# Optimization experiments

Hardware: AMD Instinct MI355X
Metric: run time of the kernel (lower is better)

Reference implementation:

```python
import math
import jax, jax.numpy as jnp
import numpy as np

B, S, D, H = 2, 2048, 1024, 16


def setup_inputs() -> dict:
    key = jax.random.key(0)
    ks = jax.random.split(key, 8)
    scale = 1.0 / math.sqrt(D)
    kv_mask = jax.random.randint(ks[1], (B, S), 0, 2).astype(bool)
    kv_mask = kv_mask.at[:, 0].set(True)  # ensure at least one valid kv per batch
    return {
        "q": jax.random.normal(ks[0], (B, S, D), dtype=jnp.float32),
        "kv_mask": kv_mask,
        "Wq": jax.random.normal(ks[2], (D, D), dtype=jnp.float32) * scale,
        "Wk": jax.random.normal(ks[3], (D, D), dtype=jnp.float32) * scale,
        "Wv": jax.random.normal(ks[4], (D, D), dtype=jnp.float32) * scale,
        "Wo": jax.random.normal(ks[5], (D, D), dtype=jnp.float32) * scale,
        "bo": jax.random.normal(ks[6], (D,), dtype=jnp.float32) * 0.01,
        "num_heads": H,
    }


def _pass_with_mask(x, W, mask, b=None):
    # Linear applied everywhere, output zeroed where mask is False (pass_with_mask)
    y = x @ W.T
    if b is not None:
        y = y + b
    return jnp.where(mask[..., None], y, 0.0)


def reference(q, kv_mask, Wq, Wk, Wv, Wo, bo, num_heads):
    b, s, d = q.shape
    hd = d // num_heads
    q_mask = jnp.ones((b, s), dtype=bool)  # default q_mask in the module
    # self-attention: k = v = q
    qh = _pass_with_mask(q, Wq, q_mask).reshape(b, s, num_heads, hd)
    kh = _pass_with_mask(q, Wk, kv_mask).reshape(b, s, num_heads, hd)
    vh = _pass_with_mask(q, Wv, kv_mask).reshape(b, s, num_heads, hd)
    # scores: note the module scales by sqrt(model_dim), NOT sqrt(head_dim)
    scores = jnp.einsum("bqhd,bkhd->bhqk", qh, kh) / math.sqrt(d)
    mask = (q_mask[:, :, None] & kv_mask[:, None, :])[:, None, :, :]  # [b,1,q,k]
    scores = jnp.where(mask, scores, -jnp.inf)
    attn = jax.nn.softmax(scores, axis=-1)
    attn = jnp.where(mask, attn, 0.0)
    out = jnp.einsum("bhqk,bkhd->bqhd", attn, vh).reshape(b, s, d)
    return _pass_with_mask(out, Wo, q_mask, bo)
```

## Files before the change

### kernel.cpp

```cpp
#include <hip/hip_runtime.h>
#include <math.h>

#define B_ 2
#define S_ 2048
#define DM 1024
#define NH 16
#define HD 64

typedef unsigned short u16;
typedef unsigned int u32;
typedef __attribute__((ext_vector_type(8))) short bf16x8;
typedef __attribute__((ext_vector_type(4))) float f32x4;

#define C2SCALE 0.0450842200277800f

__device__ __forceinline__ u16 f2bf(float x) {
  unsigned u = __float_as_uint(x);
  u = (u + 0x7FFFu + ((u >> 16) & 1u)) >> 16;
  return (u16)u;
}

__device__ __forceinline__ u32 cvtpk(float lo, float hi) {
  u32 r;
  asm("v_cvt_pk_bf16_f32 %0, %1, %2" : "=v"(r) : "v"(lo), "v"(hi));
  return r;
}

__device__ __forceinline__ float exp2a(float x) {
  float r;
  asm("v_exp_f32 %0, %1" : "=v"(r) : "v"(x));
  return r;
}

__device__ __forceinline__ void gload_lds16(const u16* g, u16* l) {
  __builtin_amdgcn_global_load_lds((const __attribute__((address_space(1))) void*)g,
                                   (__attribute__((address_space(3))) void*)l, 16, 0, 0);
}

__device__ __forceinline__ int sigpos(int w6) {
  return ((w6 >> 5) << 5) | (((w6 >> 2) & 3) << 3) | (((w6 >> 4) & 1) << 2) | (w6 & 3);
}

__global__ void cvt_all(const float* __restrict__ q, const float* __restrict__ Wq,
                        const float* __restrict__ Wk, const float* __restrict__ Wv,
                        const float* __restrict__ Wo, const int* __restrict__ kvm,
                        u16* __restrict__ Xbf, u16* __restrict__ Wcat,
                        u16* __restrict__ Wobf, u16* __restrict__ mwg) {
  const int NQ4 = (B_ * S_ * DM) / 4;
  const int NW4 = (DM * DM) / 4;
  const int total = NQ4 + 4 * NW4;
  int i = blockIdx.x * blockDim.x + threadIdx.x;
  int stride = gridDim.x * blockDim.x;
  for (int t = i; t < B_ * S_; t += stride) {
    int kv = t & (S_ - 1);
    mwg[(t & ~(S_ - 1)) + (kv & ~63) + sigpos(kv & 63)] = kvm[t] ? 0xFFFFu : 0u;
  }
  for (; i < total; i += stride) {
    const float* src;
    u16* dst;
    if (i < NQ4) {
      src = q + (size_t)i * 4; dst = Xbf + (size_t)i * 4;
    } else {
      int t = i - NQ4;
      if (t < NW4)            { src = Wq + (size_t)t * 4; dst = Wcat + (size_t)t * 4; }
      else if (t < 2 * NW4)   { src = Wk + (size_t)(t - NW4) * 4;     dst = Wcat + DM * DM + (size_t)(t - NW4) * 4; }
      else if (t < 3 * NW4)   { src = Wv + (size_t)(t - 2 * NW4) * 4; dst = Wcat + 2 * DM * DM + (size_t)(t - 2 * NW4) * 4; }
      else                    { src = Wo + (size_t)(t - 3 * NW4) * 4; dst = Wobf + (size_t)(t - 3 * NW4) * 4; }
    }
    float4 v = *(const float4*)src;
    ushort4 o;
    o.x = f2bf(v.x); o.y = f2bf(v.y); o.z = f2bf(v.z); o.w = f2bf(v.w);
    *(ushort4*)dst = o;
  }
}

template <int MODE>
__global__ __launch_bounds__(256, 2) void gemm_bt(
    const u16* __restrict__ A, const u16* __restrict__ Bw, int K,
    u16* __restrict__ qo, u16* __restrict__ ko, u16* __restrict__ vo,
    float* __restrict__ fo, const float* __restrict__ bias, int N) {
  __shared__ __align__(16) u16 As[128 * 32];
  __shared__ __align__(16) u16 Bs[128 * 32];
  const int tid = threadIdx.x;
  const int wv = tid >> 6, lane = tid & 63;
  const int g = lane >> 4, c = lane & 15;
  const int wr = wv >> 1, wc = wv & 1;
  const int L = blockIdx.y * gridDim.x + blockIdx.x;
  const int cpx = (gridDim.x * gridDim.y) >> 3;
  const int Ls = (L & 7) * cpx + (L >> 3);
  const int Mb = (Ls & 31) << 7, Nb = (Ls >> 5) << 7;

  f32x4 acc[4][4];
#pragma unroll
  for (int i = 0; i < 4; i++)
#pragma unroll
    for (int j = 0; j < 4; j++) acc[i][j] = f32x4{0.f, 0.f, 0.f, 0.f};

  for (int kb = 0; kb < K; kb += 32) {
#pragma unroll
    for (int it = 0; it < 2; ++it) {
      int id = it * 256 + tid;
      int m = id >> 2, kk = (id & 3) * 8;
      gload_lds16(A + (size_t)(Mb + m) * K + kb + kk, As + (it * 4 + wv) * 512);
      gload_lds16(Bw + (size_t)(Nb + m) * K + kb + kk, Bs + (it * 4 + wv) * 512);
    }
    __syncthreads();
    bf16x8 af[4], bfr[4];
#pragma unroll
    for (int mi = 0; mi < 4; mi++)
      af[mi] = *(const bf16x8*)(As + (wr * 64 + mi * 16 + c) * 32 + g * 8);
#pragma unroll
    for (int ni = 0; ni < 4; ni++)
      bfr[ni] = *(const bf16x8*)(Bs + (wc * 64 + ni * 16 + c) * 32 + g * 8);
#pragma unroll
    for (int mi = 0; mi < 4; mi++)
#pragma unroll
      for (int ni = 0; ni < 4; ni++)
        acc[mi][ni] = __builtin_amdgcn_mfma_f32_16x16x32_bf16(af[mi], bfr[ni], acc[mi][ni], 0, 0, 0);
    __syncthreads();
  }

  if (MODE == 0) {
#pragma unroll
    for (int mi = 0; mi < 4; mi++) {
#pragma unroll
      for (int ni = 0; ni < 4; ni++) {
        int n = Nb + wc * 64 + ni * 16 + c;
        int which = n >> 10, nn = n & 1023;
        int h = nn >> 6, d = nn & 63;
        int row0 = Mb + wr * 64 + mi * 16 + g * 4;
        int b0 = row0 >> 11, s0 = row0 & 2047;
        if (which == 2) {
          int pos = sigpos(s0 & 63);
          uint2 o;
          o.x = cvtpk(acc[mi][ni][0], acc[mi][ni][1]);
          o.y = cvtpk(acc[mi][ni][2], acc[mi][ni][3]);
          *(uint2*)(vo + ((size_t)((b0 * NH + h) * HD + d)) * S_ + (s0 & ~63) + pos) = o;
        } else if (which == 0) {
#pragma unroll
          for (int r = 0; r < 4; r++)
            qo[(((size_t)(b0 * NH + h)) * S_ + s0 + r) * HD + d] =
                f2bf(acc[mi][ni][r] * C2SCALE);
        } else {
#pragma unroll
          for (int r = 0; r < 4; r++)
            ko[(((size_t)(b0 * NH + h)) * S_ + s0 + r) * HD + d] = f2bf(acc[mi][ni][r]);
        }
      }
    }
  } else {
#pragma unroll
    for (int mi = 0; mi < 4; mi++) {
#pragma unroll
      for (int ni = 0; ni < 4; ni++) {
        int n = Nb + wc * 64 + ni * 16 + c;
        float bv = bias[n];
#pragma unroll
        for (int r = 0; r < 4; r++) {
          int row = Mb + wr * 64 + mi * 16 + g * 4 + r;
          fo[(size_t)row * N + n] = acc[mi][ni][r] + bv;
        }
      }
    }
  }
}

__global__ __launch_bounds__(512, 4) void attn_kernel(
    const u16* __restrict__ qb, const u16* __restrict__ kb,
    const u16* __restrict__ vtb, const u16* __restrict__ mwg,
    u16* __restrict__ ob) {
  __shared__ __align__(16) u16 Kl[2][64 * 64];
  __shared__ __align__(16) u16 Vl[2][64 * 64];
  __shared__ __align__(16) u16 MW[S_];

  const int tid = threadIdx.x;
  const int wv = tid >> 6, lane = tid & 63;
  const int g = lane >> 4, c = lane & 15;

  const int L = blockIdx.x;
  const int j = L >> 3;
  const int bh = ((L & 7) << 2) | (j >> 4);
  const int qi = j & 15;
  const int b = bh >> 4, h = bh & 15;
  const int q0 = qi * 128;
  const size_t bhbase = (size_t)bh * (S_ * HD);

  ((uint2*)MW)[tid] = ((const uint2*)(mwg + b * S_))[tid];

  bf16x8 qf[2];
#pragma unroll
  for (int ks = 0; ks < 2; ks++)
    qf[ks] = *(const bf16x8*)(qb + bhbase + (size_t)(q0 + wv * 16 + c) * HD + ks * 32 + g * 8);

  f32x4 Oa[4];
#pragma unroll
  for (int di = 0; di < 4; di++) Oa[di] = f32x4{0.f, 0.f, 0.f, 0.f};
  f32x4 lacc = f32x4{0.f, 0.f, 0.f, 0.f};

  union { u32 u[4]; bf16x8 v; } ones;
#pragma unroll
  for (int w = 0; w < 4; w++) ones.u[w] = 0x3F803F80u;

  const int srow = tid >> 3;
  const int scol8 = tid & 7;
  const u16* kg = kb + bhbase + (size_t)srow * HD + scol8 * 8;
  const u16* vg = vtb + bhbase + (size_t)srow * S_ + scol8 * 8;
  const int wslot = scol8 ^ (srow & 7);
  u16* kld = &Kl[0][srow * 64 + wslot * 8];
  u16* vld = &Vl[0][srow * 64 + wslot * 8];

  bf16x8 krg = *(const bf16x8*)kg;
  bf16x8 vrg = *(const bf16x8*)vg;
  *(bf16x8*)kld = krg;
  *(bf16x8*)vld = vrg;
  krg = *(const bf16x8*)(kg + 64 * HD);
  vrg = *(const bf16x8*)(vg + 64);
  __syncthreads();

  const int swz = c & 7;
  const int NT = 32;

  for (int t = 0; t < NT; ++t) {
    const int cur = t & 1;
    if (t + 1 < NT) {
      *(bf16x8*)(kld + (cur ^ 1) * 4096) = krg;
      *(bf16x8*)(vld + (cur ^ 1) * 4096) = vrg;
      if (t + 2 < NT) {
        krg = *(const bf16x8*)(kg + (t + 2) * (64 * HD));
        vrg = *(const bf16x8*)(vg + (t + 2) * 64);
      }
    }
    const u16* KB = &Kl[cur][0];
    const u16* VB = &Vl[cur][0];

    f32x4 Sa[4];
#pragma unroll
    for (int ni = 0; ni < 4; ni++) Sa[ni] = f32x4{0.f, 0.f, 0.f, 0.f};
    __builtin_amdgcn_s_setprio(1);
#pragma unroll
    for (int ks = 0; ks < 2; ks++) {
      bf16x8 kf[4];
#pragma unroll
      for (int ni = 0; ni < 4; ni++)
        kf[ni] = *(const bf16x8*)&KB[(ni * 16 + c) * 64 + (((4 * ks + g) ^ swz) * 8)];
#pragma unroll
      for (int ni = 0; ni < 4; ni++)
        Sa[ni] = __builtin_amdgcn_mfma_f32_16x16x32_bf16(kf[ni], qf[ks], Sa[ni], 0, 0, 0);
    }
    __builtin_amdgcn_s_setprio(0);

    bf16x8 Pa[2];
#pragma unroll
    for (int ks = 0; ks < 2; ks++) {
      uint4 mw = *(const uint4*)&MW[t * 64 + ks * 32 + g * 8];
      union { u32 u[4]; bf16x8 v; } pw;
      pw.u[0] = cvtpk(exp2a(Sa[2 * ks][0]), exp2a(Sa[2 * ks][1])) & mw.x;
      pw.u[1] = cvtpk(exp2a(Sa[2 * ks][2]), exp2a(Sa[2 * ks][3])) & mw.y;
      pw.u[2] = cvtpk(exp2a(Sa[2 * ks + 1][0]), exp2a(Sa[2 * ks + 1][1])) & mw.z;
      pw.u[3] = cvtpk(exp2a(Sa[2 * ks + 1][2]), exp2a(Sa[2 * ks + 1][3])) & mw.w;
      Pa[ks] = pw.v;
    }

    __builtin_amdgcn_s_setprio(1);
    lacc = __builtin_amdgcn_mfma_f32_16x16x32_bf16(ones.v, Pa[0], lacc, 0, 0, 0);
    lacc = __builtin_amdgcn_mfma_f32_16x16x32_bf16(ones.v, Pa[1], lacc, 0, 0, 0);
#pragma unroll
    for (int ks = 0; ks < 2; ks++) {
      bf16x8 vf[4];
#pragma unroll
      for (int di = 0; di < 4; di++)
        vf[di] = *(const bf16x8*)&VB[(di * 16 + c) * 64 + (((4 * ks + g) ^ swz) * 8)];
#pragma unroll
      for (int di = 0; di < 4; di++)
        Oa[di] = __builtin_amdgcn_mfma_f32_16x16x32_bf16(vf[di], Pa[ks], Oa[di], 0, 0, 0);
    }
    __builtin_amdgcn_s_setprio(0);

    __syncthreads();
  }

  float inv = 1.f / lacc[0];
  int q = q0 + wv * 16 + c;
  size_t base = ((size_t)(b * S_ + q)) * DM + (size_t)h * HD;
#pragma unroll
  for (int di = 0; di < 4; di++) {
    uint2 o;
    o.x = cvtpk(Oa[di][0] * inv, Oa[di][1] * inv);
    o.y = cvtpk(Oa[di][2] * inv, Oa[di][3] * inv);
    *(uint2*)(ob + base + di * 16 + g * 4) = o;
  }
}

extern "C" void kernel_launch(void* const* d_in, const int* in_sizes, int n_in,
                              void* d_out, int out_size, void* d_ws, size_t ws_size,
                              hipStream_t stream) {
  const float* q  = (const float*)d_in[0];
  const int* kvm  = (const int*)d_in[1];
  const float* Wq = (const float*)d_in[2];
  const float* Wk = (const float*)d_in[3];
  const float* Wv = (const float*)d_in[4];
  const float* Wo = (const float*)d_in[5];
  const float* bo = (const float*)d_in[6];
  float* out = (float*)d_out;
  char* ws = (char*)d_ws;

  u16* Xbf   = (u16*)(ws);
  u16* Wcat  = (u16*)(ws + (8u << 20));
  u16* Wobf  = (u16*)(ws + (14u << 20));
  u16* qbuf  = (u16*)(ws + (16u << 20));
  u16* kbuf  = (u16*)(ws + (24u << 20));
  u16* vtbuf = (u16*)(ws + (32u << 20));
  u16* mwg   = (u16*)(ws + (40u << 20));
  u16* obuf  = Xbf;

  cvt_all<<<2048, 256, 0, stream>>>(q, Wq, Wk, Wv, Wo, kvm, Xbf, Wcat, Wobf, mwg);
  gemm_bt<0><<<dim3(32, 24), 256, 0, stream>>>(Xbf, Wcat, DM, qbuf, kbuf, vtbuf,
                                               nullptr, nullptr, 3 * DM);
  attn_kernel<<<512, 512, 0, stream>>>(qbuf, kbuf, vtbuf, mwg, obuf);
  gemm_bt<1><<<dim3(32, 8), 256, 0, stream>>>(obuf, Wobf, DM, nullptr, nullptr,
                                              nullptr, out, bo, DM);
}
```

Baseline: 113.9 us.

## Double attention KV tile to 128 keys and split output GEMM into 128x64 tiles

The attention kernel now stages 128-key K/V tiles per iteration (16 iterations instead of 32), halving the number of barriers and pipeline steps while doubling LDS per buffer. The output projection gets a dedicated 128x64-tile GEMM with 512 blocks instead of 256 128x128 blocks, giving more blocks to fill the CUs on the small final GEMM. The cost is higher LDS use per attention block, which may reduce occupancy, and more register pressure from eight score accumulators.

Result: no change. 112.2 us (-1.5%).

```diff
diff --git a/kernel.cpp b/kernel.cpp
--- a/kernel.cpp
+++ b/kernel.cpp
@@ -74,11 +74,9 @@
   }
 }
 
-template <int MODE>
 __global__ __launch_bounds__(256, 2) void gemm_bt(
     const u16* __restrict__ A, const u16* __restrict__ Bw, int K,
-    u16* __restrict__ qo, u16* __restrict__ ko, u16* __restrict__ vo,
-    float* __restrict__ fo, const float* __restrict__ bias, int N) {
+    u16* __restrict__ qo, u16* __restrict__ ko, u16* __restrict__ vo) {
   __shared__ __align__(16) u16 As[128 * 32];
   __shared__ __align__(16) u16 Bs[128 * 32];
   const int tid = threadIdx.x;
@@ -120,46 +118,92 @@
     __syncthreads();
   }
 
-  if (MODE == 0) {
-#pragma unroll
-    for (int mi = 0; mi < 4; mi++) {
-#pragma unroll
-      for (int ni = 0; ni < 4; ni++) {
-        int n = Nb + wc * 64 + ni * 16 + c;
-        int which = n >> 10, nn = n & 1023;
-        int h = nn >> 6, d = nn & 63;
-        int row0 = Mb + wr * 64 + mi * 16 + g * 4;
-        int b0 = row0 >> 11, s0 = row0 & 2047;
-        if (which == 2) {
-          int pos = sigpos(s0 & 63);
-          uint2 o;
-          o.x = cvtpk(acc[mi][ni][0], acc[mi][ni][1]);
-          o.y = cvtpk(acc[mi][ni][2], acc[mi][ni][3]);
-          *(uint2*)(vo + ((size_t)((b0 * NH + h) * HD + d)) * S_ + (s0 & ~63) + pos) = o;
-        } else if (which == 0) {
-#pragma unroll
-          for (int r = 0; r < 4; r++)
-            qo[(((size_t)(b0 * NH + h)) * S_ + s0 + r) * HD + d] =
-                f2bf(acc[mi][ni][r] * C2SCALE);
-        } else {
-#pragma unroll
-          for (int r = 0; r < 4; r++)
-            ko[(((size_t)(b0 * NH + h)) * S_ + s0 + r) * HD + d] = f2bf(acc[mi][ni][r]);
-        }
-      }
-    }
-  } else {
-#pragma unroll
-    for (int mi = 0; mi < 4; mi++) {
-#pragma unroll
-      for (int ni = 0; ni < 4; ni++) {
-        int n = Nb + wc * 64 + ni * 16 + c;
-        float bv = bias[n];
-#pragma unroll
-        for (int r = 0; r < 4; r++) {
-          int row = Mb + wr * 64 + mi * 16 + g * 4 + r;
-          fo[(size_t)row * N + n] = acc[mi][ni][r] + bv;
-        }
+#pragma unroll
+  for (int mi = 0; mi < 4; mi++) {
+#pragma unroll
+    for (int ni = 0; ni < 4; ni++) {
+      int n = Nb + wc * 64 + ni * 16 + c;
+      int which = n >> 10, nn = n & 1023;
+      int h = nn >> 6, d = nn & 63;
+      int row0 = Mb + wr * 64 + mi * 16 + g * 4;
+      int b0 = row0 >> 11, s0 = row0 & 2047;
+      if (which == 2) {
+        int pos = sigpos(s0 & 63);
+        uint2 o;
+        o.x = cvtpk(acc[mi][ni][0], acc[mi][ni][1]);
+        o.y = cvtpk(acc[mi][ni][2], acc[mi][ni][3]);
+        *(uint2*)(vo + ((size_t)((b0 * NH + h) * HD + d)) * S_ + (s0 & ~63) + pos) = o;
+      } else if (which == 0) {
+#pragma unroll
+        for (int r = 0; r < 4; r++)
+          qo[(((size_t)(b0 * NH + h)) * S_ + s0 + r) * HD + d] =
+              f2bf(acc[mi][ni][r] * C2SCALE);
+      } else {
+#pragma unroll
+        for (int r = 0; r < 4; r++)
+          ko[(((size_t)(b0 * NH + h)) * S_ + s0 + r) * HD + d] = f2bf(acc[mi][ni][r]);
+      }
+    }
+  }
+}
+
+__global__ __launch_bounds__(256, 4) void gemm_n64(
+    const u16* __restrict__ A, const u16* __restrict__ Bw,
+    const float* __restrict__ bias, float* __restrict__ fo) {
+  __shared__ __align__(16) u16 As[128 * 32];
+  __shared__ __align__(16) u16 Bs[64 * 32];
+  const int K = DM, N = DM;
+  const int tid = threadIdx.x;
+  const int wv = tid >> 6, lane = tid & 63;
+  const int g = lane >> 4, c = lane & 15;
+  const int wr = wv >> 1, wc = wv & 1;
+  const int L = blockIdx.x;
+  const int Ls = (L & 7) * 64 + (L >> 3);
+  const int Mb = (Ls & 31) << 7, Nb = (Ls >> 5) << 6;
+
+  f32x4 acc[4][2];
+#pragma unroll
+  for (int i = 0; i < 4; i++)
+#pragma unroll
+    for (int j = 0; j < 2; j++) acc[i][j] = f32x4{0.f, 0.f, 0.f, 0.f};
+
+  for (int kb = 0; kb < K; kb += 32) {
+#pragma unroll
+    for (int it = 0; it < 2; ++it) {
+      int id = it * 256 + tid;
+      int m = id >> 2, kk = (id & 3) * 8;
+      gload_lds16(A + (size_t)(Mb + m) * K + kb + kk, As + (it * 4 + wv) * 512);
+    }
+    {
+      int m = tid >> 2, kk = (tid & 3) * 8;
+      gload_lds16(Bw + (size_t)(Nb + m) * K + kb + kk, Bs + wv * 512);
+    }
+    __syncthreads();
+    bf16x8 af[4], bfr[2];
+#pragma unroll
+    for (int mi = 0; mi < 4; mi++)
+      af[mi] = *(const bf16x8*)(As + (wr * 64 + mi * 16 + c) * 32 + g * 8);
+#pragma unroll
+    for (int ni = 0; ni < 2; ni++)
+      bfr[ni] = *(const bf16x8*)(Bs + (wc * 32 + ni * 16 + c) * 32 + g * 8);
+#pragma unroll
+    for (int mi = 0; mi < 4; mi++)
+#pragma unroll
+      for (int ni = 0; ni < 2; ni++)
+        acc[mi][ni] = __builtin_amdgcn_mfma_f32_16x16x32_bf16(af[mi], bfr[ni], acc[mi][ni], 0, 0, 0);
+    __syncthreads();
+  }
+
+#pragma unroll
+  for (int mi = 0; mi < 4; mi++) {
+#pragma unroll
+    for (int ni = 0; ni < 2; ni++) {
+      int n = Nb + wc * 32 + ni * 16 + c;
+      float bv = bias[n];
+#pragma unroll
+      for (int r = 0; r < 4; r++) {
+        int row = Mb + wr * 64 + mi * 16 + g * 4 + r;
+        fo[(size_t)row * N + n] = acc[mi][ni][r] + bv;
       }
     }
   }
@@ -169,8 +213,8 @@
     const u16* __restrict__ qb, const u16* __restrict__ kb,
     const u16* __restrict__ vtb, const u16* __restrict__ mwg,
     u16* __restrict__ ob) {
-  __shared__ __align__(16) u16 Kl[2][64 * 64];
-  __shared__ __align__(16) u16 Vl[2][64 * 64];
+  __shared__ __align__(16) u16 Kl[2][128 * 64];
+  __shared__ __align__(16) u16 Vl[2][64 * 128];
   __shared__ __align__(16) u16 MW[S_];
 
   const int tid = threadIdx.x;
@@ -201,78 +245,82 @@
 #pragma unroll
   for (int w = 0; w < 4; w++) ones.u[w] = 0x3F803F80u;
 
-  const int srow = tid >> 3;
-  const int scol8 = tid & 7;
-  const u16* kg = kb + bhbase + (size_t)srow * HD + scol8 * 8;
-  const u16* vg = vtb + bhbase + (size_t)srow * S_ + scol8 * 8;
-  const int wslot = scol8 ^ (srow & 7);
-  u16* kld = &Kl[0][srow * 64 + wslot * 8];
-  u16* vld = &Vl[0][srow * 64 + wslot * 8];
-
-  bf16x8 krg = *(const bf16x8*)kg;
-  bf16x8 vrg = *(const bf16x8*)vg;
-  *(bf16x8*)kld = krg;
-  *(bf16x8*)vld = vrg;
-  krg = *(const bf16x8*)(kg + 64 * HD);
-  vrg = *(const bf16x8*)(vg + 64);
+  const int kr1 = tid >> 3, kc1 = tid & 7;
+  const int vd1 = tid >> 4, vch1 = tid & 15;
+  const u16* kg1 = kb + bhbase + (size_t)kr1 * HD + kc1 * 8;
+  const u16* kg2 = kg1 + (size_t)64 * HD;
+  const u16* vg1 = vtb + bhbase + (size_t)vd1 * S_ + vch1 * 8;
+  const u16* vg2 = vg1 + (size_t)32 * S_;
+  u16* kld1 = &Kl[0][kr1 * 64 + (kc1 ^ (kr1 & 7)) * 8];
+  u16* kld2 = &Kl[0][(64 + kr1) * 64 + (kc1 ^ (kr1 & 7)) * 8];
+  u16* vld1 = &Vl[0][vd1 * 128 + (vch1 ^ (vd1 & 7)) * 8];
+  u16* vld2 = &Vl[0][(32 + vd1) * 128 + (vch1 ^ (vd1 & 7)) * 8];
+
+  bf16x8 krg[2], vrg[2];
+  krg[0] = *(const bf16x8*)kg1;  krg[1] = *(const bf16x8*)kg2;
+  vrg[0] = *(const bf16x8*)vg1;  vrg[1] = *(const bf16x8*)vg2;
+  *(bf16x8*)kld1 = krg[0];  *(bf16x8*)kld2 = krg[1];
+  *(bf16x8*)vld1 = vrg[0];  *(bf16x8*)vld2 = vrg[1];
+  krg[0] = *(const bf16x8*)(kg1 + 8192);  krg[1] = *(const bf16x8*)(kg2 + 8192);
+  vrg[0] = *(const bf16x8*)(vg1 + 128);   vrg[1] = *(const bf16x8*)(vg2 + 128);
   __syncthreads();
 
   const int swz = c & 7;
-  const int NT = 32;
+  const int NT = 16;
 
   for (int t = 0; t < NT; ++t) {
     const int cur = t & 1;
     if (t + 1 < NT) {
-      *(bf16x8*)(kld + (cur ^ 1) * 4096) = krg;
-      *(bf16x8*)(vld + (cur ^ 1) * 4096) = vrg;
+      const int nb = (cur ^ 1) * 8192;
+      *(bf16x8*)(kld1 + nb) = krg[0];  *(bf16x8*)(kld2 + nb) = krg[1];
+      *(bf16x8*)(vld1 + nb) = vrg[0];  *(bf16x8*)(vld2 + nb) = vrg[1];
       if (t + 2 < NT) {
-        krg = *(const bf16x8*)(kg + (t + 2) * (64 * HD));
-        vrg = *(const bf16x8*)(vg + (t + 2) * 64);
+        krg[0] = *(const bf16x8*)(kg1 + (t + 2) * 8192);
+        krg[1] = *(const bf16x8*)(kg2 + (t + 2) * 8192);
+        vrg[0] = *(const bf16x8*)(vg1 + (t + 2) * 128);
+        vrg[1] = *(const bf16x8*)(vg2 + (t + 2) * 128);
       }
     }
     const u16* KB = &Kl[cur][0];
     const u16* VB = &Vl[cur][0];
 
-    f32x4 Sa[4];
-#pragma unroll
-    for (int ni = 0; ni < 4; ni++) Sa[ni] = f32x4{0.f, 0.f, 0.f, 0.f};
+    f32x4 Sa[8];
+#pragma unroll
+    for (int ni = 0; ni < 8; ni++) Sa[ni] = f32x4{0.f, 0.f, 0.f, 0.f};
     __builtin_amdgcn_s_setprio(1);
 #pragma unroll
     for (int ks = 0; ks < 2; ks++) {
-      bf16x8 kf[4];
-#pragma unroll
-      for (int ni = 0; ni < 4; ni++)
-        kf[ni] = *(const bf16x8*)&KB[(ni * 16 + c) * 64 + (((4 * ks + g) ^ swz) * 8)];
-#pragma unroll
-      for (int ni = 0; ni < 4; ni++)
-        Sa[ni] = __builtin_amdgcn_mfma_f32_16x16x32_bf16(kf[ni], qf[ks], Sa[ni], 0, 0, 0);
+#pragma unroll
+      for (int ni = 0; ni < 8; ni++) {
+        bf16x8 kf = *(const bf16x8*)&KB[(ni * 16 + c) * 64 + (((4 * ks + g) ^ swz) * 8)];
+        Sa[ni] = __builtin_amdgcn_mfma_f32_16x16x32_bf16(kf, qf[ks], Sa[ni], 0, 0, 0);
+      }
     }
     __builtin_amdgcn_s_setprio(0);
 
-    bf16x8 Pa[2];
-#pragma unroll
-    for (int ks = 0; ks < 2; ks++) {
-      uint4 mw = *(const uint4*)&MW[t * 64 + ks * 32 + g * 8];
+    bf16x8 Pa[4];
+#pragma unroll
+    for (int kc = 0; kc < 4; kc++) {
+      uint4 mw = *(const uint4*)&MW[t * 128 + kc * 32 + g * 8];
       union { u32 u[4]; bf16x8 v; } pw;
-      pw.u[0] = cvtpk(exp2a(Sa[2 * ks][0]), exp2a(Sa[2 * ks][1])) & mw.x;
-      pw.u[1] = cvtpk(exp2a(Sa[2 * ks][2]), exp2a(Sa[2 * ks][3])) & mw.y;
-      pw.u[2] = cvtpk(exp2a(Sa[2 * ks + 1][0]), exp2a(Sa[2 * ks + 1][1])) & mw.z;
-      pw.u[3] = cvtpk(exp2a(Sa[2 * ks + 1][2]), exp2a(Sa[2 * ks + 1][3])) & mw.w;
-      Pa[ks] = pw.v;
+      pw.u[0] = cvtpk(exp2a(Sa[2 * kc][0]), exp2a(Sa[2 * kc][1])) & mw.x;
+      pw.u[1] = cvtpk(exp2a(Sa[2 * kc][2]), exp2a(Sa[2 * kc][3])) & mw.y;
+      pw.u[2] = cvtpk(exp2a(Sa[2 * kc + 1][0]), exp2a(Sa[2 * kc + 1][1])) & mw.z;
+      pw.u[3] = cvtpk(exp2a(Sa[2 * kc + 1][2]), exp2a(Sa[2 * kc + 1][3])) & mw.w;
+      Pa[kc] = pw.v;
     }
 
     __builtin_amdgcn_s_setprio(1);
-    lacc = __builtin_amdgcn_mfma_f32_16x16x32_bf16(ones.v, Pa[0], lacc, 0, 0, 0);
-    lacc = __builtin_amdgcn_mfma_f32_16x16x32_bf16(ones.v, Pa[1], lacc, 0, 0, 0);
-#pragma unroll
-    for (int ks = 0; ks < 2; ks++) {
-      bf16x8 vf[4];
-#pragma unroll
-      for (int di = 0; di < 4; di++)
-        vf[di] = *(const bf16x8*)&VB[(di * 16 + c) * 64 + (((4 * ks + g) ^ swz) * 8)];
-#pragma unroll
-      for (int di = 0; di < 4; di++)
-        Oa[di] = __builtin_amdgcn_mfma_f32_16x16x32_bf16(vf[di], Pa[ks], Oa[di], 0, 0, 0);
+#pragma unroll
+    for (int kc = 0; kc < 4; kc++)
+      lacc = __builtin_amdgcn_mfma_f32_16x16x32_bf16(ones.v, Pa[kc], lacc, 0, 0, 0);
+#pragma unroll
+    for (int kc = 0; kc < 4; kc++) {
+#pragma unroll
+      for (int di = 0; di < 4; di++) {
+        bf16x8 vf = *(const bf16x8*)&VB[(di * 16 + c) * 128 + (((4 * kc + g) ^ swz) * 8)];
+        Oa[di] = __builtin_amdgcn_mfma_f32_16x16x32_bf16(vf, Pa[kc], Oa[di], 0, 0, 0);
+      }
     }
     __builtin_amdgcn_s_setprio(0);
 
@@ -314,9 +362,7 @@
   u16* obuf  = Xbf;
 
   cvt_all<<<2048, 256, 0, stream>>>(q, Wq, Wk, Wv, Wo, kvm, Xbf, Wcat, Wobf, mwg);
-  gemm_bt<0><<<dim3(32, 24), 256, 0, stream>>>(Xbf, Wcat, DM, qbuf, kbuf, vtbuf,
-                                               nullptr, nullptr, 3 * DM);
+  gemm_bt<<<dim3(32, 24), 256, 0, stream>>>(Xbf, Wcat, DM, qbuf, kbuf, vtbuf);
   attn_kernel<<<512, 512, 0, stream>>>(qbuf, kbuf, vtbuf, mwg, obuf);
-  gemm_bt<1><<<dim3(32, 8), 256, 0, stream>>>(obuf, Wobf, DM, nullptr, nullptr,
-                                              nullptr, out, bo, DM);
-}
+  gemm_n64<<<512, 256, 0, stream>>>(obuf, Wobf, bo, out);
+}
```
